# Kernel optimization log

Measured on AMD Instinct MI355X. Metric: run time of the kernel, lower is better.

## Reference

```python
import jax, jax.numpy as jnp
import numpy as np

B, T, D = 2, 2048, 1024
H = 16
HD = D // H

def setup_inputs() -> dict:
    key = jax.random.key(0)
    ks = jax.random.split(key, 5)
    s = 1.0 / np.sqrt(D)
    return {
        "x": jax.random.normal(ks[0], (B, T, D), dtype=jnp.float32),
        "Wq": jax.random.normal(ks[1], (D, D), dtype=jnp.float32) * s,
        "bq": jnp.zeros((D,), jnp.float32),
        "Wk": jax.random.normal(ks[2], (D, D), dtype=jnp.float32) * s,
        "bk": jnp.zeros((D,), jnp.float32),
        "Wv": jax.random.normal(ks[3], (D, D), dtype=jnp.float32) * s,
        "bv": jnp.zeros((D,), jnp.float32),
        "Wo": jax.random.normal(ks[4], (D, D), dtype=jnp.float32) * s,
        "bo": jnp.zeros((D,), jnp.float32),
    }

def reference(x, Wq, bq, Wk, bk, Wv, bv, Wo, bo):
    # projections: torch Linear computes x @ W.T + b
    def split_heads(t):  # [B,T,D] -> [B,H,T,HD]
        return t.reshape(B, T, H, HD).transpose(0, 2, 1, 3)
    q = split_heads(x @ Wq.T + bq)
    k = split_heads(x @ Wk.T + bk)
    v = split_heads(x @ Wv.T + bv)
    scale = 1.0 / jnp.sqrt(jnp.asarray(HD, x.dtype))
    scores = jnp.einsum("bhtd,bhsd->bhts", q, k) * scale  # [B,H,T,T]
    causal = jnp.tril(jnp.ones((T, T), bool))
    scores = jnp.where(causal, scores, -jnp.inf)
    attn = jax.nn.softmax(scores, axis=-1)
    out = jnp.einsum("bhts,bhsd->bhtd", attn, v)  # [B,H,T,HD]
    out = out.transpose(0, 2, 1, 3).reshape(B, T, D)
    return out @ Wo.T + bo
```

## Files before the change

### kernel.cpp

```cpp
#include <hip/hip_runtime.h>
#include <hip/hip_bf16.h>

#define B_NUM 2
#define T_LEN 2048
#define D_DIM 1024
#define H_NUM 16
#define HD_DIM 64

using bf16x8 = __attribute__((ext_vector_type(8))) short;
using f32x4  = __attribute__((ext_vector_type(4))) float;
using u16x4  = __attribute__((ext_vector_type(4))) unsigned short;

__device__ __forceinline__ unsigned short f2bf(float f) {
    union { __hip_bfloat16 b; unsigned short u; } v;
    v.b = __float2bfloat16(f);
    return v.u;
}

__device__ __forceinline__ void gload16(const unsigned short* g, unsigned short* l) {
    __builtin_amdgcn_global_load_lds(
        (const __attribute__((address_space(1))) void*)g,
        (__attribute__((address_space(3))) void*)l, 16, 0, 0);
}

__global__ __launch_bounds__(256) void cvt5(
    const float* __restrict__ s0, const float* __restrict__ s1, const float* __restrict__ s2,
    const float* __restrict__ s3, const float* __restrict__ s4,
    unsigned short* __restrict__ d0, unsigned short* __restrict__ d1, unsigned short* __restrict__ d2,
    unsigned short* __restrict__ d3, unsigned short* __restrict__ d4,
    int c0, int c1, int c2, int c3, int c4)
{
    const float* src; unsigned short* dst; int cnt;
    switch (blockIdx.z) {
        case 0: src = s0; dst = d0; cnt = c0; break;
        case 1: src = s1; dst = d1; cnt = c1; break;
        case 2: src = s2; dst = d2; cnt = c2; break;
        case 3: src = s3; dst = d3; cnt = c3; break;
        default: src = s4; dst = d4; cnt = c4; break;
    }
    const int stride = gridDim.x * 256 * 4;
    for (int i = (blockIdx.x * 256 + threadIdx.x) * 4; i < cnt; i += stride) {
        float4 v = *(const float4*)(src + i);
        u16x4 o = { f2bf(v.x), f2bf(v.y), f2bf(v.z), f2bf(v.w) };
        *(u16x4*)(dst + i) = o;
    }
}

__device__ __forceinline__ void tile128(
    const unsigned short* __restrict__ A, const unsigned short* __restrict__ Bm,
    int m0, int n0, int K, unsigned short* lds, f32x4 acc[4][4])
{
    const int tid  = threadIdx.x;
    const int lane = tid & 63, w = tid >> 6;
    const int g = lane >> 4, c = lane & 15;
    const int wr = w >> 1, wc = w & 1;
    const int srow = lane >> 2;
    const int sch  = lane & 3;
    const int scsw = sch ^ ((srow >> 1) & 3);
    const int chunk = w * 2;
    const int row0 = chunk * 16 + srow;
    const int row1 = row0 + 16;
    const int rsw = (c >> 1) & 3;

    #pragma unroll
    for (int mi = 0; mi < 4; ++mi)
        #pragma unroll
        for (int ni = 0; ni < 4; ++ni)
            acc[mi][ni] = (f32x4){0.f, 0.f, 0.f, 0.f};

    const unsigned short* gA0 = A  + (size_t)(m0 + row0) * K + scsw * 8;
    const unsigned short* gA1 = A  + (size_t)(m0 + row1) * K + scsw * 8;
    const unsigned short* gB0 = Bm + (size_t)(n0 + row0) * K + scsw * 8;
    const unsigned short* gB1 = Bm + (size_t)(n0 + row1) * K + scsw * 8;

    auto stage = [&](int buf, int k0) {
        unsigned short* bA = lds + buf * 8192;
        unsigned short* bB = bA + 4096;
        gload16(gA0 + k0, bA + chunk * 512);
        gload16(gA1 + k0, bA + (chunk + 1) * 512);
        gload16(gB0 + k0, bB + chunk * 512);
        gload16(gB1 + k0, bB + (chunk + 1) * 512);
    };

    auto kstep = [&](int buf) {
        __builtin_amdgcn_s_barrier();
        asm volatile("" ::: "memory");
        const unsigned short* bA = lds + buf * 8192;
        const unsigned short* bB = bA + 4096;
        bf16x8 af[4], bfr[4];
        #pragma unroll
        for (int mi = 0; mi < 4; ++mi)
            af[mi] = *(const bf16x8*)(bA + (wr * 64 + mi * 16 + c) * 32 + (g ^ rsw) * 8);
        #pragma unroll
        for (int ni = 0; ni < 4; ++ni)
            bfr[ni] = *(const bf16x8*)(bB + (wc * 64 + ni * 16 + c) * 32 + (g ^ rsw) * 8);
        #pragma unroll
        for (int mi = 0; mi < 4; ++mi)
            #pragma unroll
            for (int ni = 0; ni < 4; ++ni)
                acc[mi][ni] = __builtin_amdgcn_mfma_f32_16x16x32_bf16(af[mi], bfr[ni], acc[mi][ni], 0, 0, 0);
        asm volatile("s_waitcnt lgkmcnt(0)" ::: "memory");
        __builtin_amdgcn_s_barrier();
    };

    const int nsteps = K / 32;
    stage(0, 0);
    stage(1, 32);
    int buf = 0;
    #pragma unroll 1
    for (int t = 0; t + 2 < nsteps; ++t) {
        int nb = buf + 2; if (nb >= 3) nb -= 3;
        stage(nb, (t + 2) * 32);
        asm volatile("s_waitcnt vmcnt(8)" ::: "memory");
        kstep(buf);
        ++buf; if (buf == 3) buf = 0;
    }
    asm volatile("s_waitcnt vmcnt(4)" ::: "memory");
    kstep(buf);
    ++buf; if (buf == 3) buf = 0;
    asm volatile("s_waitcnt vmcnt(0)" ::: "memory");
    kstep(buf);
}

__global__ __launch_bounds__(256) void gemm_qkv(
    const unsigned short* __restrict__ X,
    const unsigned short* __restrict__ Wq, const unsigned short* __restrict__ Wk,
    const unsigned short* __restrict__ Wv,
    const float* __restrict__ bq, const float* __restrict__ bk, const float* __restrict__ bv,
    unsigned short* __restrict__ Oq, unsigned short* __restrict__ Ok, unsigned short* __restrict__ OvT)
{
    __shared__ __align__(16) unsigned short lds[3 * 8192];
    const int bsw = (blockIdx.x & 7) * 96 + (blockIdx.x >> 3);
    const int mt = bsw / 24;
    const int rr = bsw - mt * 24;
    const int z  = rr >> 3;
    const int nt = rr & 7;

    const int lane = threadIdx.x & 63, w = threadIdx.x >> 6;
    const int g = lane >> 4, c = lane & 15;
    const int wr = w >> 1, wc = w & 1;
    f32x4 acc[4][4];

    if (z < 2) {
        const unsigned short* W = z ? Wk : Wq;
        const float* bias       = z ? bk : bq;
        unsigned short* Ob      = z ? Ok : Oq;
        const int m0 = mt * 128, n0 = nt * 128;
        tile128(X, W, m0, n0, D_DIM, lds, acc);
        #pragma unroll
        for (int mi = 0; mi < 4; ++mi) {
            #pragma unroll
            for (int ni = 0; ni < 4; ++ni) {
                const int col = n0 + wc * 64 + ni * 16 + c;
                const int h = col >> 6, hd = col & 63;
                const float bb = bias[col];
                #pragma unroll
                for (int r = 0; r < 4; ++r) {
                    const int row = m0 + wr * 64 + mi * 16 + g * 4 + r;
                    const int b_ = row >> 11, t = row & (T_LEN - 1);
                    Ob[((size_t)((b_ * H_NUM + h) * T_LEN + t)) * HD_DIM + hd] = f2bf(acc[mi][ni][r] + bb);
                }
            }
        }
    } else {
        const int m0 = nt * 128, n0 = mt * 128;
        tile128(Wv, X, m0, n0, D_DIM, lds, acc);
        #pragma unroll
        for (int mi = 0; mi < 4; ++mi) {
            #pragma unroll
            for (int ni = 0; ni < 4; ++ni) {
                const int j = n0 + wc * 64 + ni * 16 + c;
                const int b_ = j >> 11, t = j & (T_LEN - 1);
                #pragma unroll
                for (int r = 0; r < 4; ++r) {
                    const int f = m0 + wr * 64 + mi * 16 + g * 4 + r;
                    OvT[(size_t)(b_ * D_DIM + f) * T_LEN + t] = f2bf(acc[mi][ni][r] + bv[f]);
                }
            }
        }
    }
}

__global__ __launch_bounds__(256) void gemm_out(
    const unsigned short* __restrict__ A, const unsigned short* __restrict__ W,
    const float* __restrict__ bias, float* __restrict__ Out)
{
    __shared__ __align__(16) unsigned short lds[3 * 8192];
    const int bsw = (blockIdx.x & 7) * 32 + (blockIdx.x >> 3);
    const int mt = bsw >> 3, nt = bsw & 7;
    const int lane = threadIdx.x & 63, w = threadIdx.x >> 6;
    const int g = lane >> 4, c = lane & 15;
    const int m0 = mt * 128, n0 = nt * 128;
    f32x4 acc[4][4];
    tile128(A, W, m0, n0, D_DIM, lds, acc);
    const int wr = w >> 1, wc = w & 1;
    #pragma unroll
    for (int mi = 0; mi < 4; ++mi) {
        #pragma unroll
        for (int ni = 0; ni < 4; ++ni) {
            const int col = n0 + wc * 64 + ni * 16 + c;
            const float bb = bias[col];
            #pragma unroll
            for (int r = 0; r < 4; ++r) {
                const int row = m0 + wr * 64 + mi * 16 + g * 4 + r;
                Out[(size_t)row * D_DIM + col] = acc[mi][ni][r] + bb;
            }
        }
    }
}

__global__ __launch_bounds__(256, 4) void attn(
    const unsigned short* __restrict__ Q, const unsigned short* __restrict__ K,
    const unsigned short* __restrict__ VT, unsigned short* __restrict__ O)
{
    __shared__ __align__(16) unsigned short kv_lds[2][2][64 * 64];
    __shared__ __align__(16) unsigned short plbuf[4][16 * 64];
    const int tid = threadIdx.x, lane = tid & 63, w = tid >> 6;
    const int g = lane >> 4, c = lane & 15;

    const int gid = blockIdx.x;
    const int bh = gid & 31;
    const int jt = (gid < 512) ? (31 - (gid >> 5)) : ((gid - 512) >> 5);
    const int q0b = jt * 64;
    const int qw0 = q0b + w * 16;

    const unsigned short* Qb = Q  + (size_t)bh * T_LEN * HD_DIM;
    const unsigned short* Kb = K  + (size_t)bh * T_LEN * HD_DIM;
    const unsigned short* Vb = VT + (size_t)bh * HD_DIM * T_LEN;
    unsigned short* pl = plbuf[w];

    bf16x8 qf[2];
    #pragma unroll
    for (int kk = 0; kk < 2; ++kk)
        qf[kk] = *(const bf16x8*)(Qb + (size_t)(qw0 + c) * HD_DIM + kk * 32 + g * 8);

    f32x4 acc[4];
    #pragma unroll
    for (int ni = 0; ni < 4; ++ni) acc[ni] = (f32x4){0.f, 0.f, 0.f, 0.f};
    float m2 = -1e30f, l2 = 0.f;

    auto stage = [&](int buf, int kv0) {
        unsigned short* kb = &kv_lds[buf][0][0];
        unsigned short* vb = &kv_lds[buf][1][0];
        #pragma unroll
        for (int rnd = 0; rnd < 2; ++rnd) {
            const int bch = rnd * 256 + w * 64;
            const int row = (bch >> 3) + (lane >> 3);
            const int sc16 = (lane & 7) ^ (row & 7);
            gload16(Kb + (size_t)(kv0 + row) * HD_DIM + sc16 * 8, kb + bch * 8);
            gload16(Vb + (size_t)row * T_LEN + kv0 + sc16 * 8,   vb + bch * 8);
        }
    };

    const int ntiles = jt + 1;
    stage(0, 0);
    __syncthreads();
    int cur = 0;
    #pragma unroll 1
    for (int t = 0; t < ntiles; ++t) {
        const int kv0 = t << 6;
        if (t + 1 < ntiles) stage(cur ^ 1, kv0 + 64);
        const unsigned short* kb = &kv_lds[cur][0][0];
        const unsigned short* vb = &kv_lds[cur][1][0];

        f32x4 sf[4];
        #pragma unroll
        for (int st = 0; st < 4; ++st) {
            const int rr = st * 16 + c;
            bf16x8 kf0 = *(const bf16x8*)(kb + rr * 64 + ((g       ^ (c & 7)) * 8));
            bf16x8 kf1 = *(const bf16x8*)(kb + rr * 64 + (((4 + g) ^ (c & 7)) * 8));
            f32x4 s = (f32x4){0.f, 0.f, 0.f, 0.f};
            s = __builtin_amdgcn_mfma_f32_16x16x32_bf16(kf0, qf[0], s, 0, 0, 0);
            s = __builtin_amdgcn_mfma_f32_16x16x32_bf16(kf1, qf[1], s, 0, 0, 0);
            sf[st] = s;
        }
        if (t == jt) {
            const int qg = qw0 + c;
            #pragma unroll
            for (int st = 0; st < 4; ++st)
                #pragma unroll
                for (int r = 0; r < 4; ++r) {
                    const int kvg = kv0 + st * 16 + g * 4 + r;
                    sf[st][r] = (kvg <= qg) ? sf[st][r] * 0.125f : -1e30f;
                }
        } else {
            #pragma unroll
            for (int st = 0; st < 4; ++st)
                #pragma unroll
                for (int r = 0; r < 4; ++r)
                    sf[st][r] *= 0.125f;
        }
        float mx = sf[0][0];
        #pragma unroll
        for (int st = 0; st < 4; ++st)
            #pragma unroll
            for (int r = 0; r < 4; ++r) mx = fmaxf(mx, sf[st][r]);
        mx = fmaxf(mx, __shfl_xor(mx, 16));
        mx = fmaxf(mx, __shfl_xor(mx, 32));
        if (__any(mx > m2 + 8.f)) {
            const float mnew = fmaxf(m2, mx);
            const float alpha = __expf(m2 - mnew);
            float ar[4];
            #pragma unroll
            for (int r = 0; r < 4; ++r) ar[r] = __shfl(alpha, g * 4 + r);
            l2 *= alpha;
            #pragma unroll
            for (int ni = 0; ni < 4; ++ni)
                #pragma unroll
                for (int r = 0; r < 4; ++r) acc[ni][r] *= ar[r];
            m2 = mnew;
        }
        float sum = 0.f;
        #pragma unroll
        for (int st = 0; st < 4; ++st)
            #pragma unroll
            for (int r = 0; r < 4; ++r) {
                const float p = __expf(sf[st][r] - m2);
                sf[st][r] = p;
                sum += p;
            }
        sum += __shfl_xor(sum, 16);
        sum += __shfl_xor(sum, 32);
        l2 += sum;
        #pragma unroll
        for (int st = 0; st < 4; ++st) {
            const unsigned lo = ((unsigned)f2bf(sf[st][1]) << 16) | f2bf(sf[st][0]);
            const unsigned hi = ((unsigned)f2bf(sf[st][3]) << 16) | f2bf(sf[st][2]);
            uint2 pk; pk.x = lo; pk.y = hi;
            const int idx = (c * 64 + st * 16 + g * 4) ^ ((c & 7) << 3);
            *(uint2*)(pl + idx) = pk;
        }
        asm volatile("" ::: "memory");
        bf16x8 pa[2];
        #pragma unroll
        for (int kk = 0; kk < 2; ++kk) {
            const int ridx = (c * 64 + kk * 32 + g * 8) ^ ((c & 7) << 3);
            pa[kk] = *(const bf16x8*)(pl + ridx);
        }
        #pragma unroll
        for (int ni = 0; ni < 4; ++ni) {
            const int rr = ni * 16 + c;
            bf16x8 vf0 = *(const bf16x8*)(vb + rr * 64 + ((g       ^ (c & 7)) * 8));
            bf16x8 vf1 = *(const bf16x8*)(vb + rr * 64 + (((4 + g) ^ (c & 7)) * 8));
            acc[ni] = __builtin_amdgcn_mfma_f32_16x16x32_bf16(pa[0], vf0, acc[ni], 0, 0, 0);
            acc[ni] = __builtin_amdgcn_mfma_f32_16x16x32_bf16(pa[1], vf1, acc[ni], 0, 0, 0);
        }
        __syncthreads();
        cur ^= 1;
    }

    const float linv = 1.0f / l2;
    float lr[4];
    #pragma unroll
    for (int r = 0; r < 4; ++r) lr[r] = __shfl(linv, g * 4 + r);
    const int b_ = bh >> 4, h = bh & 15;
    #pragma unroll
    for (int ni = 0; ni < 4; ++ni)
        #pragma unroll
        for (int r = 0; r < 4; ++r) {
            const int q = qw0 + g * 4 + r;
            O[(size_t)(b_ * T_LEN + q) * D_DIM + h * HD_DIM + ni * 16 + c] =
                f2bf(acc[ni][r] * lr[r]);
        }
}

extern "C" void kernel_launch(void* const* d_in, const int* in_sizes, int n_in,
                              void* d_out, int out_size, void* d_ws, size_t ws_size,
                              hipStream_t stream)
{
    const float* x  = (const float*)d_in[0];
    const float* Wq = (const float*)d_in[1];
    const float* bq = (const float*)d_in[2];
    const float* Wk = (const float*)d_in[3];
    const float* bk = (const float*)d_in[4];
    const float* Wv = (const float*)d_in[5];
    const float* bv = (const float*)d_in[6];
    const float* Wo = (const float*)d_in[7];
    const float* bo = (const float*)d_in[8];
    float* out = (float*)d_out;

    char* ws = (char*)d_ws;
    const size_t MB = 1u << 20;
    unsigned short* xb  = (unsigned short*)(ws + 0 * MB);
    unsigned short* wqb = (unsigned short*)(ws + 8 * MB);
    unsigned short* wkb = (unsigned short*)(ws + 10 * MB);
    unsigned short* wvb = (unsigned short*)(ws + 12 * MB);
    unsigned short* wob = (unsigned short*)(ws + 14 * MB);
    unsigned short* qw  = (unsigned short*)(ws + 16 * MB);
    unsigned short* kw  = (unsigned short*)(ws + 24 * MB);
    unsigned short* vtw = (unsigned short*)(ws + 32 * MB);
    unsigned short* ow  = (unsigned short*)(ws + 40 * MB);

    cvt5<<<dim3(1024, 1, 5), dim3(256), 0, stream>>>(
        x, Wq, Wk, Wv, Wo, xb, wqb, wkb, wvb, wob,
        B_NUM * T_LEN * D_DIM, D_DIM * D_DIM, D_DIM * D_DIM, D_DIM * D_DIM, D_DIM * D_DIM);

    gemm_qkv<<<dim3(768), dim3(256), 0, stream>>>(
        xb, wqb, wkb, wvb, bq, bk, bv, qw, kw, vtw);

    attn<<<dim3(1024), dim3(256), 0, stream>>>(qw, kw, vtw, ow);

    gemm_out<<<dim3(256), dim3(256), 0, stream>>>(
        ow, wob, bo, out);
}
```

Measured before the change: 108.4 us.

## Prefetch KV two tiles ahead with vmcnt waits; fold softmax scale into Q

Restructures the attention KV pipeline so two tiles are in flight. Explicit s_waitcnt vmcnt plus raw barriers replace __syncthreads, and the next-next tile is issued after the MMA loop. The Q projection now prescales by log2(e)/sqrt(HD), so the per-score multiply goes away and exp2 replaces __expf. It also tree-reduces the row max and packs pairs with a bf16x2 conversion. The hand-counted vmcnt and the barrier ordering risk a race if the load count assumptions are wrong.

```diff
diff --git a/kernel.cpp b/kernel.cpp
--- a/kernel.cpp
+++ b/kernel.cpp
@@ -7,6 +7,8 @@
 #define H_NUM 16
 #define HD_DIM 64
 
+#define Q_PRESCALE 0.18033688011112042f
+
 using bf16x8 = __attribute__((ext_vector_type(8))) short;
 using f32x4  = __attribute__((ext_vector_type(4))) float;
 using u16x4  = __attribute__((ext_vector_type(4))) unsigned short;
@@ -14,6 +16,12 @@
 __device__ __forceinline__ unsigned short f2bf(float f) {
     union { __hip_bfloat16 b; unsigned short u; } v;
     v.b = __float2bfloat16(f);
+    return v.u;
+}
+
+__device__ __forceinline__ unsigned pack2bf(float a, float b) {
+    union { __hip_bfloat162 h; unsigned u; } v;
+    v.h = __float22bfloat162_rn(float2{a, b});
     return v.u;
 }
 
@@ -145,6 +153,7 @@
         const unsigned short* W = z ? Wk : Wq;
         const float* bias       = z ? bk : bq;
         unsigned short* Ob      = z ? Ok : Oq;
+        const float oscale      = z ? 1.0f : Q_PRESCALE;
         const int m0 = mt * 128, n0 = nt * 128;
         tile128(X, W, m0, n0, D_DIM, lds, acc);
         #pragma unroll
@@ -158,7 +167,8 @@
                 for (int r = 0; r < 4; ++r) {
                     const int row = m0 + wr * 64 + mi * 16 + g * 4 + r;
                     const int b_ = row >> 11, t = row & (T_LEN - 1);
-                    Ob[((size_t)((b_ * H_NUM + h) * T_LEN + t)) * HD_DIM + hd] = f2bf(acc[mi][ni][r] + bb);
+                    Ob[((size_t)((b_ * H_NUM + h) * T_LEN + t)) * HD_DIM + hd] =
+                        f2bf((acc[mi][ni][r] + bb) * oscale);
                 }
             }
         }
@@ -254,12 +264,16 @@
 
     const int ntiles = jt + 1;
     stage(0, 0);
-    __syncthreads();
+    if (ntiles > 1) stage(1, 64);
     int cur = 0;
     #pragma unroll 1
     for (int t = 0; t < ntiles; ++t) {
         const int kv0 = t << 6;
-        if (t + 1 < ntiles) stage(cur ^ 1, kv0 + 64);
+        if (t + 1 < ntiles)
+            asm volatile("s_waitcnt vmcnt(4)" ::: "memory");
+        else
+            asm volatile("s_waitcnt vmcnt(0)" ::: "memory");
+        __builtin_amdgcn_s_barrier();
         const unsigned short* kb = &kv_lds[cur][0][0];
         const unsigned short* vb = &kv_lds[cur][1][0];
 
@@ -281,25 +295,20 @@
                 #pragma unroll
                 for (int r = 0; r < 4; ++r) {
                     const int kvg = kv0 + st * 16 + g * 4 + r;
-                    sf[st][r] = (kvg <= qg) ? sf[st][r] * 0.125f : -1e30f;
+                    sf[st][r] = (kvg <= qg) ? sf[st][r] : -1e30f;
                 }
-        } else {
-            #pragma unroll
-            for (int st = 0; st < 4; ++st)
-                #pragma unroll
-                for (int r = 0; r < 4; ++r)
-                    sf[st][r] *= 0.125f;
-        }
-        float mx = sf[0][0];
-        #pragma unroll
-        for (int st = 0; st < 4; ++st)
-            #pragma unroll
-            for (int r = 0; r < 4; ++r) mx = fmaxf(mx, sf[st][r]);
+        }
+        float ma = fmaxf(fmaxf(sf[0][0], sf[0][1]), sf[0][2]);
+        float mb = fmaxf(fmaxf(sf[0][3], sf[1][0]), sf[1][1]);
+        float mc = fmaxf(fmaxf(sf[1][2], sf[1][3]), sf[2][0]);
+        float md = fmaxf(fmaxf(sf[2][1], sf[2][2]), sf[2][3]);
+        float me = fmaxf(fmaxf(sf[3][0], sf[3][1]), sf[3][2]);
+        float mx = fmaxf(fmaxf(fmaxf(ma, mb), fmaxf(mc, md)), fmaxf(me, sf[3][3]));
         mx = fmaxf(mx, __shfl_xor(mx, 16));
         mx = fmaxf(mx, __shfl_xor(mx, 32));
         if (__any(mx > m2 + 8.f)) {
             const float mnew = fmaxf(m2, mx);
-            const float alpha = __expf(m2 - mnew);
+            const float alpha = __builtin_amdgcn_exp2f(m2 - mnew);
             float ar[4];
             #pragma unroll
             for (int r = 0; r < 4; ++r) ar[r] = __shfl(alpha, g * 4 + r);
@@ -315,7 +324,7 @@
         for (int st = 0; st < 4; ++st)
             #pragma unroll
             for (int r = 0; r < 4; ++r) {
-                const float p = __expf(sf[st][r] - m2);
+                const float p = __builtin_amdgcn_exp2f(sf[st][r] - m2);
                 sf[st][r] = p;
                 sum += p;
             }
@@ -324,9 +333,9 @@
         l2 += sum;
         #pragma unroll
         for (int st = 0; st < 4; ++st) {
-            const unsigned lo = ((unsigned)f2bf(sf[st][1]) << 16) | f2bf(sf[st][0]);
-            const unsigned hi = ((unsigned)f2bf(sf[st][3]) << 16) | f2bf(sf[st][2]);
-            uint2 pk; pk.x = lo; pk.y = hi;
+            uint2 pk;
+            pk.x = pack2bf(sf[st][0], sf[st][1]);
+            pk.y = pack2bf(sf[st][2], sf[st][3]);
             const int idx = (c * 64 + st * 16 + g * 4) ^ ((c & 7) << 3);
             *(uint2*)(pl + idx) = pk;
         }
@@ -345,7 +354,9 @@
             acc[ni] = __builtin_amdgcn_mfma_f32_16x16x32_bf16(pa[0], vf0, acc[ni], 0, 0, 0);
             acc[ni] = __builtin_amdgcn_mfma_f32_16x16x32_bf16(pa[1], vf1, acc[ni], 0, 0, 0);
         }
-        __syncthreads();
+        asm volatile("s_waitcnt lgkmcnt(0)" ::: "memory");
+        __builtin_amdgcn_s_barrier();
+        if (t + 2 < ntiles) stage(cur, (t + 2) << 6);
         cur ^= 1;
     }
 
```

Result: faster. 101.8 us (-6.1%).
